# Kernel tuning notes

Measured on AMD Instinct MI355X. Metric: run time of the kernel, lower is better.

Reference implementation:

```python
import jax, jax.numpy as jnp
import numpy as np

H = 8
D = 512
DK = D // H  # 64
ALPHA = 0.2  # leaky relu negative slope


def setup_inputs() -> dict:
    key = jax.random.key(0)
    ks = jax.random.split(key, 10)
    B, N = 8, 1024
    query = jax.random.normal(ks[0], (B, N, D), dtype=jnp.float32)
    key_t = jax.random.normal(ks[1], (B, N, D), dtype=jnp.float32)
    value = jax.random.normal(ks[2], (B, N, D), dtype=jnp.float32)
    mask = jax.random.randint(ks[3], (B, N, N), 0, 2, dtype=jnp.int32)
    scale = 0.02
    Wq = jax.random.normal(ks[4], (D, D), dtype=jnp.float32) * scale
    Wk = jax.random.normal(ks[5], (D, D), dtype=jnp.float32) * scale
    Wv = jax.random.normal(ks[6], (D, D), dtype=jnp.float32) * scale
    Wo = jax.random.normal(ks[7], (D, D), dtype=jnp.float32) * scale
    bq = jnp.zeros((D,), jnp.float32)
    bk = jnp.zeros((D,), jnp.float32)
    bv = jnp.zeros((D,), jnp.float32)
    bo = jnp.zeros((D,), jnp.float32)
    # xavier-uniform-like init for the attention vector a: shape (h, 2*d_k)
    limit = float(np.sqrt(6.0 / (H + 2 * DK)))
    a = jax.random.uniform(ks[8], (H, 2 * DK), dtype=jnp.float32, minval=-limit, maxval=limit)
    return {"query": query, "key": key_t, "value": value, "mask": mask,
            "Wq": Wq, "bq": bq, "Wk": Wk, "bk": bk, "Wv": Wv, "bv": bv,
            "Wo": Wo, "bo": bo, "a": a}


def reference(query, key, value, mask, Wq, bq, Wk, bk, Wv, bv, Wo, bo, a):
    B, N, _ = query.shape

    def proj(x, W, b):
        # torch Linear: x @ W.T + b, then split heads -> (B, H, N, DK)
        return (x @ W.T + b).reshape(B, N, H, DK).transpose(0, 2, 1, 3)

    q = proj(query, Wq, bq)
    k = proj(key, Wk, bk)
    v = proj(value, Wv, bv)

    # 'cat' attention: scores[b,h,i,j] = concat(q_i, k_j) . a[h]
    #                = q_i . a[h,:DK] + k_j . a[h,DK:]  (algebraic decomposition,
    #                 avoids the O(N^2 * 2*DK) concat tensor of the torch code)
    sq = jnp.einsum('bhnd,hd->bhn', q, a[:, :DK])
    sk = jnp.einsum('bhnd,hd->bhn', k, a[:, DK:])
    scores = sq[:, :, :, None] + sk[:, :, None, :]  # (B, H, N, N)

    # mask == 0 -> -inf (mask broadcast over heads), applied BEFORE leaky relu
    scores = jnp.where(mask[:, None, :, :] == 0, -jnp.inf, scores)
    # leaky relu (leaky_relu(-inf) == -inf, preserved)
    scores = jnp.where(scores >= 0, scores, ALPHA * scores)

    p = jax.nn.softmax(scores, axis=-1)
    # fully-masked rows produce NaN -> replace with 0 (as in the torch code)
    p = jnp.where(jnp.isnan(p), jnp.zeros_like(p), p)

    x = jnp.einsum('bhnm,bhmd->bhnd', p, v)
    x = x.transpose(0, 2, 1, 3).reshape(B, N, D)
    return x @ Wo.T + bo
```

## Files before the change

### kernel.cpp

```cpp
#include <hip/hip_runtime.h>
#include <hip/hip_bf16.h>
#include <stdint.h>


typedef __attribute__((ext_vector_type(8))) short short8;
typedef __attribute__((ext_vector_type(4))) float f32x4;

#define LB __launch_bounds__(256)

union U8 { unsigned u[4]; short8 s; uint4 v; };
union U2 { unsigned u[2]; uint2 v; };

__device__ __forceinline__ unsigned short f2bf(float f) {
  unsigned int u = __float_as_uint(f);
  u += 0x7fffu + ((u >> 16) & 1u);
  return (unsigned short)(u >> 16);
}

__device__ __forceinline__ unsigned cvt_pk(float a, float b) {
  unsigned r;
  asm("v_cvt_pk_bf16_f32 %0, %1, %2" : "=v"(r) : "v"(a), "v"(b));
  return r;
}

__device__ __forceinline__ void async_cp16(const void* g, void* l) {
  __builtin_amdgcn_global_load_lds(
      (const __attribute__((address_space(1))) unsigned int*)g,
      (__attribute__((address_space(3))) unsigned int*)l, 16, 0, 0);
}

__global__ LB void prep_kernel(const float* __restrict__ Wv, const float* __restrict__ Wo,
                               unsigned short* __restrict__ wv16, unsigned short* __restrict__ wo16,
                               const float* __restrict__ Wq, const float* __restrict__ Wk,
                               const float* __restrict__ a, const float* __restrict__ bq,
                               const float* __restrict__ bk,
                               unsigned short* __restrict__ Bfrag, float* __restrict__ qkb) {
  const int blk = blockIdx.x, tid = threadIdx.x;
  if (blk < 512) {
    const float* src = blk < 256 ? Wv : Wo;
    unsigned short* dst = blk < 256 ? wv16 : wo16;
    const int idx = ((blk & 255) * 256 + tid) * 4;
    const float4 v = *(const float4*)(src + idx);
    U2 pk;
    pk.u[0] = cvt_pk(v.x, v.y);
    pk.u[1] = cvt_pk(v.z, v.w);
    *(uint2*)(dst + idx) = pk.v;
    return;
  }
  const int t = (blk - 512) * 256 + tid;
  const int d = t & 511, h = t >> 9;
  float aq = 0.f, ak = 0.f;
#pragma unroll 4
  for (int dk = 0; dk < 64; ++dk) {
    aq += Wq[(size_t)(h * 64 + dk) * 512 + d] * a[h * 128 + dk];
    ak += Wk[(size_t)(h * 64 + dk) * 512 + d] * a[h * 128 + 64 + dk];
  }
  const float L2E = 1.4426950408889634f;
  const int ks = d >> 5, lch = (d >> 3) & 3, tt = d & 7;
  Bfrag[((ks * 64 + (lch << 4) + h) << 3) + tt] = f2bf(aq * L2E);
  Bfrag[((ks * 64 + (lch << 4) + 8 + h) << 3) + tt] = f2bf(ak * L2E);
  if (d == 0) {
    float s1 = 0.f, s2 = 0.f;
    for (int dk = 0; dk < 64; ++dk) {
      s1 += bq[h * 64 + dk] * a[h * 128 + dk];
      s2 += bk[h * 64 + dk] * a[h * 128 + 64 + dk];
    }
    qkb[h] = s1 * L2E;
    qkb[8 + h] = s2 * L2E;
  }
}

__global__ LB void mid_kernel(const float* __restrict__ query, const float* __restrict__ key,
                              const unsigned short* __restrict__ Bfrag,
                              const float* __restrict__ qkb,
                              float* __restrict__ sq, float* __restrict__ sk,
                              const float* __restrict__ value,
                              const unsigned short* __restrict__ wv16,
                              const float* __restrict__ bvb, unsigned short* __restrict__ vt,
                              const int* __restrict__ mask, unsigned int* __restrict__ bits) {
  __shared__ char sm[20480];
  const int tid = threadIdx.x, w = tid >> 6, l = tid & 63;
  const int lr = l & 15, lc = l >> 4;
  const int bid = blockIdx.x;
  if (bid >= 1536) {
    unsigned char* nb = (unsigned char*)sm;
    const size_t e0 = ((size_t)(bid - 1536) * 256 + tid) * 4;
    const int4 m = *(const int4*)(mask + e0);
    nb[tid] = (unsigned char)((m.x != 0) | ((m.y != 0) << 1) | ((m.z != 0) << 2) | ((m.w != 0) << 3));
    __syncthreads();
    if (tid < 32) {
      const uint2 p = *(const uint2*)(nb + tid * 8);
      const unsigned lo = p.x, hi = p.y;
      const unsigned wl = (lo & 0xFu) | ((lo >> 4) & 0xF0u) | ((lo >> 8) & 0xF00u) | ((lo >> 12) & 0xF000u);
      const unsigned wh = (hi & 0xFu) | ((hi >> 4) & 0xF0u) | ((hi >> 8) & 0xF00u) | ((hi >> 12) & 0xF000u);
      bits[(bid - 1536) * 32 + tid] = wl | (wh << 16);
    }
    return;
  }
  if (bid >= 1024) {
    float* comb = (float*)sm;
    const int m0 = (bid - 1024) * 16;
    const int k0 = w * 128;
    short8 bf[4];
#pragma unroll
    for (int ks = 0; ks < 4; ++ks)
      bf[ks] = *(const short8*)(Bfrag + (((w * 4 + ks) * 64 + l) << 3));
    const float* qbase = query + (size_t)(m0 + lr) * 512 + k0 + (lc << 3);
    const float* kbase = key + (size_t)(m0 + lr) * 512 + k0 + (lc << 3);
    f32x4 cq = {}, ck = {};
#pragma unroll
    for (int ks = 0; ks < 4; ++ks) {
      const float4 q0 = *(const float4*)(qbase + ks * 32);
      const float4 q1 = *(const float4*)(qbase + ks * 32 + 4);
      const float4 k0v = *(const float4*)(kbase + ks * 32);
      const float4 k1v = *(const float4*)(kbase + ks * 32 + 4);
      U8 aq, ak;
      aq.u[0] = cvt_pk(q0.x, q0.y); aq.u[1] = cvt_pk(q0.z, q0.w);
      aq.u[2] = cvt_pk(q1.x, q1.y); aq.u[3] = cvt_pk(q1.z, q1.w);
      ak.u[0] = cvt_pk(k0v.x, k0v.y); ak.u[1] = cvt_pk(k0v.z, k0v.w);
      ak.u[2] = cvt_pk(k1v.x, k1v.y); ak.u[3] = cvt_pk(k1v.z, k1v.w);
      cq = __builtin_amdgcn_mfma_f32_16x16x32_bf16(aq.s, bf[ks], cq, 0, 0, 0);
      ck = __builtin_amdgcn_mfma_f32_16x16x32_bf16(ak.s, bf[ks], ck, 0, 0, 0);
    }
    if (w) {
      float* p = comb + ((w - 1) * 64 + l) * 9;
#pragma unroll
      for (int r = 0; r < 4; ++r) { p[r] = cq[r]; p[4 + r] = ck[r]; }
    }
    __syncthreads();
    if (w == 0) {
#pragma unroll
      for (int j = 0; j < 3; ++j) {
        const float* p = comb + (j * 64 + l) * 9;
#pragma unroll
        for (int r = 0; r < 4; ++r) { cq[r] += p[r]; ck[r] += p[4 + r]; }
      }
      const int col = l & 15;
      const int mbase = m0 + (lc << 2);
      const int b = mbase >> 10;
      const float bia = qkb[col];
      if (col < 8) {
        float* out = sq + ((size_t)b * 8 + col) * 1024;
#pragma unroll
        for (int r = 0; r < 4; ++r) out[(mbase + r) & 1023] = cq[r] + bia;
      } else {
        float* out = sk + ((size_t)b * 8 + (col - 8)) * 1024;
#pragma unroll
        for (int r = 0; r < 4; ++r) out[(mbase + r) & 1023] = ck[r] + bia;
      }
    }
    return;
  }
  unsigned short* As = (unsigned short*)sm;
  unsigned short* Bs = (unsigned short*)(sm + 4096);
  const int bm = bid >> 2, bn = bid & 3;
  const int m0 = bm * 32, n0 = bn * 128;
  const int wr = (w & 1) * 16, wc = (w >> 1) * 64;
  const int rch = (lc ^ ((lr >> 1) & 3)) << 3;
  const int arow = (w << 3) + (l >> 3);
  const int akc = l & 7;
  const float* asrc = value + (size_t)(m0 + arow) * 512 + (akc << 2);
  const int ach = ((akc >> 1) ^ ((arow >> 1) & 3));
  const int aoff = arow * 32 + (ach << 3) + ((akc & 1) << 2);
  const int crow = l >> 2;
  const int brow0 = (w << 4) + crow, brow1 = ((w + 4) << 4) + crow;
  const unsigned short* bsrc0 = wv16 + (size_t)(n0 + brow0) * 512 + (((l & 3) ^ ((brow0 >> 1) & 3)) << 3);
  const unsigned short* bsrc1 = wv16 + (size_t)(n0 + brow1) * 512 + (((l & 3) ^ ((brow1 >> 1) & 3)) << 3);

  f32x4 acc[4] = {};
  float4 areg = *(const float4*)(asrc);
  async_cp16(bsrc0, Bs + (w << 9));
  async_cp16(bsrc1, Bs + ((w + 4) << 9));
  {
    U2 aw;
    aw.u[0] = cvt_pk(areg.x, areg.y);
    aw.u[1] = cvt_pk(areg.z, areg.w);
    *(uint2*)(As + aoff) = aw.v;
  }
  areg = *(const float4*)(asrc + 32);
  async_cp16(bsrc0 + 32, Bs + 4096 + (w << 9));
  async_cp16(bsrc1 + 32, Bs + 4096 + ((w + 4) << 9));
  asm volatile("s_waitcnt vmcnt(3)" ::: "memory");
  asm volatile("s_waitcnt lgkmcnt(0)" ::: "memory");
  __builtin_amdgcn_sched_barrier(0);
  __builtin_amdgcn_s_barrier();
  int buf = 0;
  for (int kt = 0; kt < 16; ++kt) {
    const short8 af = *(const short8*)(As + (buf << 10) + (wr + lr) * 32 + rch);
    __builtin_amdgcn_s_setprio(1);
#pragma unroll
    for (int j = 0; j < 4; ++j) {
      const short8 bfr = *(const short8*)(Bs + (buf << 12) + (wc + j * 16 + lr) * 32 + rch);
      acc[j] = __builtin_amdgcn_mfma_f32_16x16x32_bf16(af, bfr, acc[j], 0, 0, 0);
    }
    __builtin_amdgcn_s_setprio(0);
    __builtin_amdgcn_s_barrier();
    if (kt < 15) {
      U2 aw;
      aw.u[0] = cvt_pk(areg.x, areg.y);
      aw.u[1] = cvt_pk(areg.z, areg.w);
      *(uint2*)(As + ((buf ^ 1) << 10) + aoff) = aw.v;
      if (kt < 14) {
        areg = *(const float4*)(asrc + (kt + 2) * 32);
        async_cp16(bsrc0 + (kt + 2) * 32, Bs + (buf << 12) + (w << 9));
        async_cp16(bsrc1 + (kt + 2) * 32, Bs + (buf << 12) + ((w + 4) << 9));
        asm volatile("s_waitcnt vmcnt(3)" ::: "memory");
      } else {
        asm volatile("s_waitcnt vmcnt(0)" ::: "memory");
      }
      asm volatile("s_waitcnt lgkmcnt(0)" ::: "memory");
      __builtin_amdgcn_sched_barrier(0);
      __builtin_amdgcn_s_barrier();
    }
    buf ^= 1;
  }
#pragma unroll
  for (int j = 0; j < 4; ++j) {
    const int nn = n0 + wc + j * 16 + lr;
    const float bia = bvb[nn];
    const int mm0 = m0 + wr + lc * 4;
    const int b = mm0 >> 10, t0 = mm0 & 1023;
    const int h = nn >> 6, dk = nn & 63;
    U2 pk;
    pk.u[0] = cvt_pk(acc[j][0] + bia, acc[j][1] + bia);
    pk.u[1] = cvt_pk(acc[j][2] + bia, acc[j][3] + bia);
    *(uint2*)(vt + (((size_t)((b * 8 + h) * 64 + dk)) << 10) + t0) = pk.v;
  }
}

template <int BB16>
__global__ LB void gemm_bt(const unsigned short* __restrict__ A,
                           const void* __restrict__ Bwp,
                           const float* __restrict__ bias, float* __restrict__ outp) {
  __shared__ unsigned short As[2][32 * 32];
  __shared__ unsigned short Bs[2][128 * 32];
  const int tid = threadIdx.x;
  const int w = tid >> 6, l = tid & 63;
  const int lr = l & 15, lc = l >> 4;
  const int bm = blockIdx.x >> 2, bn = blockIdx.x & 3;
  const int m0 = bm * 32, n0 = bn * 128;
  const int wr = (w & 1) * 16, wc = (w >> 1) * 64;
  const int rch = (lc ^ ((lr >> 1) & 3)) << 3;
  const int arow = (w << 3) + (l >> 2);
  const int asc = (l & 3) ^ ((arow >> 1) & 3);
  const unsigned short* asrc = A + (size_t)(m0 + arow) * 512 + (asc << 3);
  const int crow = l >> 2;
  const unsigned short* b16 = (const unsigned short*)Bwp;
  const float* b32 = (const float*)Bwp;
  const int brow0 = (w << 4) + crow, brow1 = ((w + 4) << 4) + crow;
  const unsigned short* bsrc0 = b16 + (size_t)(n0 + brow0) * 512 + (((l & 3) ^ ((brow0 >> 1) & 3)) << 3);
  const unsigned short* bsrc1 = b16 + (size_t)(n0 + brow1) * 512 + (((l & 3) ^ ((brow1 >> 1) & 3)) << 3);

  f32x4 acc[4] = {};
  if (BB16) {
    if (l < 32) async_cp16(asrc, As[0] + (w << 8));
    async_cp16(bsrc0, Bs[0] + (w << 9));
    async_cp16(bsrc1, Bs[0] + ((w + 4) << 9));
    int buf = 0;
    for (int kt = 0; kt < 16; ++kt) {
      if (kt < 15) {
        const int k1 = (kt + 1) * 32;
        if (l < 32) async_cp16(asrc + k1, As[buf ^ 1] + (w << 8));
        async_cp16(bsrc0 + k1, Bs[buf ^ 1] + (w << 9));
        async_cp16(bsrc1 + k1, Bs[buf ^ 1] + ((w + 4) << 9));
        asm volatile("s_waitcnt vmcnt(3)" ::: "memory");
      } else {
        asm volatile("s_waitcnt vmcnt(0)" ::: "memory");
      }
      __builtin_amdgcn_sched_barrier(0);
      __builtin_amdgcn_s_barrier();
      const short8 af = *(const short8*)(As[buf] + (wr + lr) * 32 + rch);
      __builtin_amdgcn_s_setprio(1);
#pragma unroll
      for (int j = 0; j < 4; ++j) {
        const short8 bfr = *(const short8*)(Bs[buf] + (wc + j * 16 + lr) * 32 + rch);
        acc[j] = __builtin_amdgcn_mfma_f32_16x16x32_bf16(af, bfr, acc[j], 0, 0, 0);
      }
      __builtin_amdgcn_s_setprio(0);
      if (kt < 15) __builtin_amdgcn_s_barrier();
      buf ^= 1;
    }
  } else {
    for (int kt = 0; kt < 16; ++kt) {
      const int k0 = kt * 32;
      if (kt) __syncthreads();
      if (l < 32) async_cp16(asrc + k0, As[0] + (w << 8));
#pragma unroll
      for (int it = 0; it < 2; ++it) {
        const int idx = it * 256 + tid;
        const int row = idx >> 2, gr = idx & 3;
        const int sch = (gr ^ ((row >> 1) & 3)) << 3;
        const float4* src = (const float4*)(b32 + (size_t)(n0 + row) * 512 + k0 + gr * 8);
        const float4 b0 = src[0], b1 = src[1];
        U8 t8;
        t8.u[0] = cvt_pk(b0.x, b0.y); t8.u[1] = cvt_pk(b0.z, b0.w);
        t8.u[2] = cvt_pk(b1.x, b1.y); t8.u[3] = cvt_pk(b1.z, b1.w);
        *(uint4*)(Bs[0] + row * 32 + sch) = t8.v;
      }
      __syncthreads();
      const short8 af = *(const short8*)(As[0] + (wr + lr) * 32 + rch);
#pragma unroll
      for (int j = 0; j < 4; ++j) {
        const short8 bfr = *(const short8*)(Bs[0] + (wc + j * 16 + lr) * 32 + rch);
        acc[j] = __builtin_amdgcn_mfma_f32_16x16x32_bf16(af, bfr, acc[j], 0, 0, 0);
      }
    }
  }
#pragma unroll
  for (int j = 0; j < 4; ++j) {
    const int nn = n0 + wc + j * 16 + lr;
    const float bia = bias[nn];
    const int mm0 = m0 + wr + lc * 4;
#pragma unroll
    for (int r = 0; r < 4; ++r)
      outp[(size_t)(mm0 + r) * 512 + nn] = acc[j][r] + bia;
  }
}

__global__ LB void attn_kernel(const float* __restrict__ sq, const float* __restrict__ sk,
                               const unsigned char* __restrict__ mbits,
                               const unsigned short* __restrict__ vt,
                               unsigned short* __restrict__ xb) {
  __shared__ char smem[53248];
  unsigned short* vts = (unsigned short*)smem;
  float* sks = (float*)(smem + 32768);
  char* mks = smem + 36864;
  const int tid = threadIdx.x;
  const int w = tid >> 6, l = tid & 63;
  const int lr = l & 15, lc = l >> 4;
  const int bid = blockIdx.x;
  const int bh = bid & 63, iblk = bid >> 6;
  const int b = bh >> 3, h = bh & 7;
  const int i0b = iblk << 7;
  const int rh = w & 1, jh = w >> 1;
  const int j0 = jh << 9;
  const float* sqp = sq + (size_t)bh * 1024;
  const float* skp = sk + (size_t)bh * 1024;
  const unsigned short* vtp = vt + ((size_t)bh << 16);
  const unsigned char* mrow = mbits + ((size_t)b << 17);

  async_cp16(skp + (w << 8) + l * 4, sks + (w << 8));
#pragma unroll
  for (int m = 0; m < 4; ++m) {
    const int row = (w << 5) + (m << 3) + (l >> 3);
    const int c = (l & 7) ^ (row & 7);
    async_cp16(mrow + (size_t)(i0b + row) * 128 + (c << 4), mks + (w << 12) + (m << 10));
  }
  const int stl = l >> 2;
  const int stc = (l & 3) ^ ((stl >> 1) & 3);
  const unsigned short* vsrc = vtp + stl * 1024 + j0 + (stc << 3);
#define STAGE(bf_, jb_)                                                        \
  {                                                                            \
    unsigned short* d_ = vts + (w << 12) + ((bf_) << 11);                      \
    const unsigned short* s_ = vsrc + (jb_);                                   \
    async_cp16(s_, d_);                                                        \
    async_cp16(s_ + 16384, d_ + 512);                                          \
    async_cp16(s_ + 32768, d_ + 1024);                                         \
    async_cp16(s_ + 49152, d_ + 1536);                                         \
  }
  STAGE(0, 0);
  float sq8[4];
#pragma unroll
  for (int t = 0; t < 4; ++t) sq8[t] = sqp[i0b + (rh << 6) + (t << 4) + lr];
  __syncthreads();

  f32x4 acc[4][4] = {};
  f32x4 accs[4] = {};
  short8 ones;
#pragma unroll
  for (int t = 0; t < 8; ++t) ones[t] = (short)0x3f80;
  const int rx = (lr & 7) << 4;
  const int vread = (lc ^ ((lr >> 1) & 3)) << 3;

  int buf = 0;
  for (int s = 0; s < 16; ++s) {
    if (s < 15) {
      STAGE(buf ^ 1, (s + 1) << 5);
      asm volatile("s_waitcnt vmcnt(4)" ::: "memory");
    } else {
      asm volatile("s_waitcnt vmcnt(0)" ::: "memory");
    }
    __builtin_amdgcn_sched_barrier(0);
    const int jb = j0 + (s << 5);
    const int qb = (jb >> 3) + lc;
    const f32x4 s0 = *(const f32x4*)(sks + jb + (lc << 3));
    const f32x4 s1 = *(const f32x4*)(sks + jb + (lc << 3) + 4);
    U8 pa[4];
#pragma unroll
    for (int t = 0; t < 4; ++t) {
      const int row = (rh << 6) + (t << 4) + lr;
      const unsigned mb = (unsigned char)mks[(row << 7) + (qb ^ rx)];
      const float sqv = sq8[t];
      float e[8];
#pragma unroll
      for (int u = 0; u < 8; ++u) {
        float sv = sqv + (u < 4 ? s0[u] : s1[u - 4]);
        sv = fmaxf(sv, 0.2f * sv);
        const float ex = __builtin_amdgcn_exp2f(sv);
        e[u] = (mb & (1u << u)) ? ex : 0.0f;
      }
      pa[t].u[0] = cvt_pk(e[0], e[1]); pa[t].u[1] = cvt_pk(e[2], e[3]);
      pa[t].u[2] = cvt_pk(e[4], e[5]); pa[t].u[3] = cvt_pk(e[6], e[7]);
    }
    const unsigned short* vbb = vts + (w << 12) + (buf << 11) + vread;
    __builtin_amdgcn_s_setprio(1);
#pragma unroll
    for (int c = 0; c < 4; ++c) {
      const short8 bv = *(const short8*)(vbb + ((c << 4) + lr) * 32);
#pragma unroll
      for (int t = 0; t < 4; ++t)
        acc[t][c] = __builtin_amdgcn_mfma_f32_16x16x32_bf16(pa[t].s, bv, acc[t][c], 0, 0, 0);
    }
#pragma unroll
    for (int t = 0; t < 4; ++t)
      accs[t] = __builtin_amdgcn_mfma_f32_16x16x32_bf16(pa[t].s, ones, accs[t], 0, 0, 0);
    __builtin_amdgcn_s_setprio(0);
    buf ^= 1;
  }
#undef STAGE

  __syncthreads();
  float* cmb = (float*)smem;
  if (jh == 1) {
    float* p = cmb + ((rh << 6) + l) * 84;
#pragma unroll
    for (int t = 0; t < 4; ++t) {
#pragma unroll
      for (int c = 0; c < 4; ++c) *(f32x4*)(p + (t * 4 + c) * 4) = acc[t][c];
      *(f32x4*)(p + 64 + t * 4) = accs[t];
    }
  }
  __syncthreads();
  if (jh == 0) {
    const float* p = cmb + ((rh << 6) + l) * 84;
#pragma unroll
    for (int t = 0; t < 4; ++t) {
#pragma unroll
      for (int c = 0; c < 4; ++c) {
        const f32x4 v = *(const f32x4*)(p + (t * 4 + c) * 4);
#pragma unroll
        for (int r = 0; r < 4; ++r) acc[t][c][r] += v[r];
      }
      const f32x4 vs = *(const f32x4*)(p + 64 + t * 4);
#pragma unroll
      for (int r = 0; r < 4; ++r) accs[t][r] += vs[r];
    }
#pragma unroll
    for (int t = 0; t < 4; ++t) {
#pragma unroll
      for (int r = 0; r < 4; ++r) {
        const float sv = accs[t][r];
        const float inv = sv > 0.0f ? 1.0f / sv : 0.0f;
        const int i = i0b + (rh << 6) + (t << 4) + (lc << 2) + r;
#pragma unroll
        for (int c = 0; c < 4; ++c)
          xb[(((size_t)(b * 1024 + i)) << 9) + h * 64 + (c << 4) + lr] =
              f2bf(acc[t][c][r] * inv);
      }
    }
  }
}

extern "C" void kernel_launch(void* const* d_in, const int* in_sizes, int n_in,
                              void* d_out, int out_size, void* d_ws, size_t ws_size,
                              hipStream_t stream) {
  const float* query = (const float*)d_in[0];
  const float* key   = (const float*)d_in[1];
  const float* value = (const float*)d_in[2];
  const int*   mask  = (const int*)d_in[3];
  const float* Wq = (const float*)d_in[4];
  const float* bq = (const float*)d_in[5];
  const float* Wk = (const float*)d_in[6];
  const float* bk = (const float*)d_in[7];
  const float* Wv = (const float*)d_in[8];
  const float* bv = (const float*)d_in[9];
  const float* Wo = (const float*)d_in[10];
  const float* bo = (const float*)d_in[11];
  const float* a  = (const float*)d_in[12];

  char* oc = (char*)d_out;
  unsigned short* vt = (unsigned short*)(oc + 0);
  unsigned int* mbits = (unsigned int*)(oc + 8388608);
  float* sqv = (float*)(oc + 9437184);
  float* skv = (float*)(oc + 9699328);
  unsigned short* Bfrag = (unsigned short*)(oc + 9961472);
  float* qkb = (float*)(oc + 9977856);
  unsigned short* wv16 = (unsigned short*)(oc + 10485760);
  unsigned short* xb = (unsigned short*)d_ws;

  const bool roomy = ws_size >= 8912896;
  unsigned short* wo16 = roomy ? (unsigned short*)((char*)d_ws + 8388608) : (unsigned short*)(oc + 11010048);

  prep_kernel<<<528, 256, 0, stream>>>(Wv, Wo, wv16, wo16, Wq, Wk, a, bq, bk, Bfrag, qkb);
  mid_kernel<<<9728, 256, 0, stream>>>(query, key, Bfrag, qkb, sqv, skv,
                                       value, wv16, bv, vt, mask, mbits);
  attn_kernel<<<512, 256, 0, stream>>>(sqv, skv, (const unsigned char*)mbits, vt, xb);
  if (roomy)
    gemm_bt<1><<<1024, 256, 0, stream>>>(xb, (const void*)wo16, bo, (float*)d_out);
  else
    gemm_bt<0><<<1024, 256, 0, stream>>>(xb, (const void*)Wo, bo, (float*)d_out);
}
```

Baseline: 81.23 us.

## Split attention blocks to 64 query rows with 4-way key split and tree reduction

Each attention block now handles 64 query rows instead of 128, and each of the four waves covers a quarter of the key dimension instead of half. The grid doubles to 1024 blocks and LDS use per block drops, which should fill more CUs and raise occupancy on the 256-CU part. The price is a two-level cross-wave reduction with extra LDS traffic and barriers, plus more redundant loads of the V tiles across blocks.

```diff
diff --git a/kernel.cpp b/kernel.cpp
--- a/kernel.cpp
+++ b/kernel.cpp
@@ -321,7 +321,7 @@
                                const unsigned char* __restrict__ mbits,
                                const unsigned short* __restrict__ vt,
                                unsigned short* __restrict__ xb) {
-  __shared__ char smem[53248];
+  __shared__ char smem[45056];
   unsigned short* vts = (unsigned short*)smem;
   float* sks = (float*)(smem + 32768);
   char* mks = smem + 36864;
@@ -331,9 +331,8 @@
   const int bid = blockIdx.x;
   const int bh = bid & 63, iblk = bid >> 6;
   const int b = bh >> 3, h = bh & 7;
-  const int i0b = iblk << 7;
-  const int rh = w & 1, jh = w >> 1;
-  const int j0 = jh << 9;
+  const int i0b = iblk << 6;
+  const int j0 = w << 8;
   const float* sqp = sq + (size_t)bh * 1024;
   const float* skp = sk + (size_t)bh * 1024;
   const unsigned short* vtp = vt + ((size_t)bh << 16);
@@ -341,10 +340,10 @@
 
   async_cp16(skp + (w << 8) + l * 4, sks + (w << 8));
 #pragma unroll
-  for (int m = 0; m < 4; ++m) {
-    const int row = (w << 5) + (m << 3) + (l >> 3);
+  for (int m = 0; m < 2; ++m) {
+    const int row = (w << 4) + (m << 3) + (l >> 3);
     const int c = (l & 7) ^ (row & 7);
-    async_cp16(mrow + (size_t)(i0b + row) * 128 + (c << 4), mks + (w << 12) + (m << 10));
+    async_cp16(mrow + (size_t)(i0b + row) * 128 + (c << 4), mks + (w << 11) + (m << 10));
   }
   const int stl = l >> 2;
   const int stc = (l & 3) ^ ((stl >> 1) & 3);
@@ -361,7 +360,7 @@
   STAGE(0, 0);
   float sq8[4];
 #pragma unroll
-  for (int t = 0; t < 4; ++t) sq8[t] = sqp[i0b + (rh << 6) + (t << 4) + lr];
+  for (int t = 0; t < 4; ++t) sq8[t] = sqp[i0b + (t << 4) + lr];
   __syncthreads();
 
   f32x4 acc[4][4] = {};
@@ -373,8 +372,8 @@
   const int vread = (lc ^ ((lr >> 1) & 3)) << 3;
 
   int buf = 0;
-  for (int s = 0; s < 16; ++s) {
-    if (s < 15) {
+  for (int s = 0; s < 8; ++s) {
+    if (s < 7) {
       STAGE(buf ^ 1, (s + 1) << 5);
       asm volatile("s_waitcnt vmcnt(4)" ::: "memory");
     } else {
@@ -388,7 +387,7 @@
     U8 pa[4];
 #pragma unroll
     for (int t = 0; t < 4; ++t) {
-      const int row = (rh << 6) + (t << 4) + lr;
+      const int row = (t << 4) + lr;
       const unsigned mb = (unsigned char)mks[(row << 7) + (qb ^ rx)];
       const float sqv = sq8[t];
       float e[8];
@@ -421,37 +420,44 @@
 
   __syncthreads();
   float* cmb = (float*)smem;
-  if (jh == 1) {
-    float* p = cmb + ((rh << 6) + l) * 84;
-#pragma unroll
-    for (int t = 0; t < 4; ++t) {
-#pragma unroll
-      for (int c = 0; c < 4; ++c) *(f32x4*)(p + (t * 4 + c) * 4) = acc[t][c];
-      *(f32x4*)(p + 64 + t * 4) = accs[t];
-    }
-  }
+#define CMB_W(B_)                                                              \
+  {                                                                            \
+    float* p = cmb + ((B_) * 64 + l) * 85;                                     \
+    _Pragma("unroll") for (int t = 0; t < 4; ++t) {                            \
+      _Pragma("unroll") for (int c = 0; c < 4; ++c)                            \
+          *(f32x4*)(p + (t * 4 + c) * 4) = acc[t][c];                          \
+      *(f32x4*)(p + 64 + t * 4) = accs[t];                                     \
+    }                                                                          \
+  }
+#define CMB_A(B_)                                                              \
+  {                                                                            \
+    const float* p = cmb + ((B_) * 64 + l) * 85;                               \
+    _Pragma("unroll") for (int t = 0; t < 4; ++t) {                            \
+      _Pragma("unroll") for (int c = 0; c < 4; ++c) {                          \
+        const f32x4 v = *(const f32x4*)(p + (t * 4 + c) * 4);                  \
+        _Pragma("unroll") for (int r = 0; r < 4; ++r) acc[t][c][r] += v[r];    \
+      }                                                                        \
+      const f32x4 vs = *(const f32x4*)(p + 64 + t * 4);                        \
+      _Pragma("unroll") for (int r = 0; r < 4; ++r) accs[t][r] += vs[r];       \
+    }                                                                          \
+  }
+  if (w == 1) CMB_W(0);
+  if (w == 3) CMB_W(1);
   __syncthreads();
-  if (jh == 0) {
-    const float* p = cmb + ((rh << 6) + l) * 84;
-#pragma unroll
-    for (int t = 0; t < 4; ++t) {
-#pragma unroll
-      for (int c = 0; c < 4; ++c) {
-        const f32x4 v = *(const f32x4*)(p + (t * 4 + c) * 4);
-#pragma unroll
-        for (int r = 0; r < 4; ++r) acc[t][c][r] += v[r];
-      }
-      const f32x4 vs = *(const f32x4*)(p + 64 + t * 4);
-#pragma unroll
-      for (int r = 0; r < 4; ++r) accs[t][r] += vs[r];
-    }
+  if (w == 0) CMB_A(0);
+  if (w == 2) CMB_A(1);
+  __syncthreads();
+  if (w == 2) CMB_W(0);
+  __syncthreads();
+  if (w == 0) {
+    CMB_A(0);
 #pragma unroll
     for (int t = 0; t < 4; ++t) {
 #pragma unroll
       for (int r = 0; r < 4; ++r) {
         const float sv = accs[t][r];
         const float inv = sv > 0.0f ? 1.0f / sv : 0.0f;
-        const int i = i0b + (rh << 6) + (t << 4) + (lc << 2) + r;
+        const int i = i0b + (t << 4) + (lc << 2) + r;
 #pragma unroll
         for (int c = 0; c < 4; ++c)
           xb[(((size_t)(b * 1024 + i)) << 9) + h * 64 + (c << 4) + lr] =
@@ -459,6 +465,8 @@
       }
     }
   }
+#undef CMB_W
+#undef CMB_A
 }
 
 extern "C" void kernel_launch(void* const* d_in, const int* in_sizes, int n_in,
@@ -494,7 +502,7 @@
   prep_kernel<<<528, 256, 0, stream>>>(Wv, Wo, wv16, wo16, Wq, Wk, a, bq, bk, Bfrag, qkb);
   mid_kernel<<<9728, 256, 0, stream>>>(query, key, Bfrag, qkb, sqv, skv,
                                        value, wv16, bv, vt, mask, mbits);
-  attn_kernel<<<512, 256, 0, stream>>>(sqv, skv, (const unsigned char*)mbits, vt, xb);
+  attn_kernel<<<1024, 256, 0, stream>>>(sqv, skv, (const unsigned char*)mbits, vt, xb);
   if (roomy)
     gemm_bt<1><<<1024, 256, 0, stream>>>(xb, (const void*)wo16, bo, (float*)d_out);
   else
```

After: 90.86 us. 1.12x slower.

## Split attention key range across eight waves with register-resident V and serial reduction

Applied to the files above, without the earlier changes.

The attention kernel now launches twice as many blocks of 512 threads, each covering 64 query rows, with every wave owning a 128-key slice. V fragments are loaded straight from global memory into registers, replacing the double-buffered LDS pipeline, so shared memory per block falls from 52KB to 21KB and occupancy should rise. The partial accumulators from the eight waves are summed through a serial loop of seven LDS write/read rounds, each with two block barriers. This adds synchronization and duplicated sq/mask work, and the register V tile adds register pressure.

```diff
diff --git a/kernel.cpp b/kernel.cpp
--- a/kernel.cpp
+++ b/kernel.cpp
@@ -7,6 +7,7 @@
 typedef __attribute__((ext_vector_type(4))) float f32x4;
 
 #define LB __launch_bounds__(256)
+#define LB512 __launch_bounds__(512)
 
 union U8 { unsigned u[4]; short8 s; uint4 v; };
 union U2 { unsigned u[2]; uint2 v; };
@@ -317,51 +318,41 @@
   }
 }
 
-__global__ LB void attn_kernel(const float* __restrict__ sq, const float* __restrict__ sk,
-                               const unsigned char* __restrict__ mbits,
-                               const unsigned short* __restrict__ vt,
-                               unsigned short* __restrict__ xb) {
-  __shared__ char smem[53248];
-  unsigned short* vts = (unsigned short*)smem;
-  float* sks = (float*)(smem + 32768);
-  char* mks = smem + 36864;
+__global__ LB512 void attn_kernel(const float* __restrict__ sq, const float* __restrict__ sk,
+                                  const unsigned char* __restrict__ mbits,
+                                  const unsigned short* __restrict__ vt,
+                                  unsigned short* __restrict__ xb) {
+  __shared__ char smem[21504];
+  float* sks = (float*)smem;
+  char* mks = smem + 4096;
   const int tid = threadIdx.x;
   const int w = tid >> 6, l = tid & 63;
   const int lr = l & 15, lc = l >> 4;
   const int bid = blockIdx.x;
   const int bh = bid & 63, iblk = bid >> 6;
   const int b = bh >> 3, h = bh & 7;
-  const int i0b = iblk << 7;
-  const int rh = w & 1, jh = w >> 1;
-  const int j0 = jh << 9;
+  const int i0b = iblk << 6;
+  const int j0 = w << 7;
   const float* sqp = sq + (size_t)bh * 1024;
   const float* skp = sk + (size_t)bh * 1024;
   const unsigned short* vtp = vt + ((size_t)bh << 16);
   const unsigned char* mrow = mbits + ((size_t)b << 17);
 
-  async_cp16(skp + (w << 8) + l * 4, sks + (w << 8));
-#pragma unroll
-  for (int m = 0; m < 4; ++m) {
-    const int row = (w << 5) + (m << 3) + (l >> 3);
+  if (w < 4) async_cp16(skp + (w << 8) + l * 4, sks + (w << 8));
+  {
+    const int row = (w << 3) + (l >> 3);
     const int c = (l & 7) ^ (row & 7);
-    async_cp16(mrow + (size_t)(i0b + row) * 128 + (c << 4), mks + (w << 12) + (m << 10));
-  }
-  const int stl = l >> 2;
-  const int stc = (l & 3) ^ ((stl >> 1) & 3);
-  const unsigned short* vsrc = vtp + stl * 1024 + j0 + (stc << 3);
-#define STAGE(bf_, jb_)                                                        \
-  {                                                                            \
-    unsigned short* d_ = vts + (w << 12) + ((bf_) << 11);                      \
-    const unsigned short* s_ = vsrc + (jb_);                                   \
-    async_cp16(s_, d_);                                                        \
-    async_cp16(s_ + 16384, d_ + 512);                                          \
-    async_cp16(s_ + 32768, d_ + 1024);                                         \
-    async_cp16(s_ + 49152, d_ + 1536);                                         \
-  }
-  STAGE(0, 0);
+    async_cp16(mrow + (size_t)(i0b + row) * 128 + (c << 4), mks + (w << 10));
+  }
+  short8 vrb[4][4];
+#pragma unroll
+  for (int c = 0; c < 4; ++c)
+#pragma unroll
+    for (int s = 0; s < 4; ++s)
+      vrb[c][s] = *(const short8*)(vtp + (size_t)(c * 16 + lr) * 1024 + j0 + s * 32 + (lc << 3));
   float sq8[4];
 #pragma unroll
-  for (int t = 0; t < 4; ++t) sq8[t] = sqp[i0b + (rh << 6) + (t << 4) + lr];
+  for (int t = 0; t < 4; ++t) sq8[t] = sqp[i0b + (t << 4) + lr];
   __syncthreads();
 
   f32x4 acc[4][4] = {};
@@ -370,17 +361,9 @@
 #pragma unroll
   for (int t = 0; t < 8; ++t) ones[t] = (short)0x3f80;
   const int rx = (lr & 7) << 4;
-  const int vread = (lc ^ ((lr >> 1) & 3)) << 3;
-
-  int buf = 0;
-  for (int s = 0; s < 16; ++s) {
-    if (s < 15) {
-      STAGE(buf ^ 1, (s + 1) << 5);
-      asm volatile("s_waitcnt vmcnt(4)" ::: "memory");
-    } else {
-      asm volatile("s_waitcnt vmcnt(0)" ::: "memory");
-    }
-    __builtin_amdgcn_sched_barrier(0);
+
+#pragma unroll
+  for (int s = 0; s < 4; ++s) {
     const int jb = j0 + (s << 5);
     const int qb = (jb >> 3) + lc;
     const f32x4 s0 = *(const f32x4*)(sks + jb + (lc << 3));
@@ -388,7 +371,7 @@
     U8 pa[4];
 #pragma unroll
     for (int t = 0; t < 4; ++t) {
-      const int row = (rh << 6) + (t << 4) + lr;
+      const int row = (t << 4) + lr;
       const unsigned mb = (unsigned char)mks[(row << 7) + (qb ^ rx)];
       const float sqv = sq8[t];
       float e[8];
@@ -402,56 +385,57 @@
       pa[t].u[0] = cvt_pk(e[0], e[1]); pa[t].u[1] = cvt_pk(e[2], e[3]);
       pa[t].u[2] = cvt_pk(e[4], e[5]); pa[t].u[3] = cvt_pk(e[6], e[7]);
     }
-    const unsigned short* vbb = vts + (w << 12) + (buf << 11) + vread;
     __builtin_amdgcn_s_setprio(1);
 #pragma unroll
-    for (int c = 0; c < 4; ++c) {
-      const short8 bv = *(const short8*)(vbb + ((c << 4) + lr) * 32);
+    for (int c = 0; c < 4; ++c)
 #pragma unroll
       for (int t = 0; t < 4; ++t)
-        acc[t][c] = __builtin_amdgcn_mfma_f32_16x16x32_bf16(pa[t].s, bv, acc[t][c], 0, 0, 0);
-    }
+        acc[t][c] = __builtin_amdgcn_mfma_f32_16x16x32_bf16(pa[t].s, vrb[c][s], acc[t][c], 0, 0, 0);
 #pragma unroll
     for (int t = 0; t < 4; ++t)
       accs[t] = __builtin_amdgcn_mfma_f32_16x16x32_bf16(pa[t].s, ones, accs[t], 0, 0, 0);
     __builtin_amdgcn_s_setprio(0);
-    buf ^= 1;
-  }
-#undef STAGE
-
+  }
+
+  float* cmb = (float*)smem;
   __syncthreads();
-  float* cmb = (float*)smem;
-  if (jh == 1) {
-    float* p = cmb + ((rh << 6) + l) * 84;
-#pragma unroll
-    for (int t = 0; t < 4; ++t) {
-#pragma unroll
-      for (int c = 0; c < 4; ++c) *(f32x4*)(p + (t * 4 + c) * 4) = acc[t][c];
-      *(f32x4*)(p + 64 + t * 4) = accs[t];
-    }
-  }
-  __syncthreads();
-  if (jh == 0) {
-    const float* p = cmb + ((rh << 6) + l) * 84;
-#pragma unroll
-    for (int t = 0; t < 4; ++t) {
-#pragma unroll
-      for (int c = 0; c < 4; ++c) {
-        const f32x4 v = *(const f32x4*)(p + (t * 4 + c) * 4);
-#pragma unroll
-        for (int r = 0; r < 4; ++r) acc[t][c][r] += v[r];
-      }
-      const f32x4 vs = *(const f32x4*)(p + 64 + t * 4);
-#pragma unroll
-      for (int r = 0; r < 4; ++r) accs[t][r] += vs[r];
-    }
+#pragma unroll 1
+  for (int src = 1; src < 8; ++src) {
+    if (w == src) {
+      float* p = cmb + l * 81;
+#pragma unroll
+      for (int t = 0; t < 4; ++t) {
+#pragma unroll
+        for (int c = 0; c < 4; ++c) *(f32x4*)(p + (t * 4 + c) * 4) = acc[t][c];
+        *(f32x4*)(p + 64 + t * 4) = accs[t];
+      }
+    }
+    __syncthreads();
+    if (w == 0) {
+      const float* p = cmb + l * 81;
+#pragma unroll
+      for (int t = 0; t < 4; ++t) {
+#pragma unroll
+        for (int c = 0; c < 4; ++c) {
+          const f32x4 v = *(const f32x4*)(p + (t * 4 + c) * 4);
+#pragma unroll
+          for (int r = 0; r < 4; ++r) acc[t][c][r] += v[r];
+        }
+        const f32x4 vs = *(const f32x4*)(p + 64 + t * 4);
+#pragma unroll
+        for (int r = 0; r < 4; ++r) accs[t][r] += vs[r];
+      }
+    }
+    __syncthreads();
+  }
+  if (w == 0) {
 #pragma unroll
     for (int t = 0; t < 4; ++t) {
 #pragma unroll
       for (int r = 0; r < 4; ++r) {
         const float sv = accs[t][r];
         const float inv = sv > 0.0f ? 1.0f / sv : 0.0f;
-        const int i = i0b + (rh << 6) + (t << 4) + (lc << 2) + r;
+        const int i = i0b + (t << 4) + (lc << 2) + r;
 #pragma unroll
         for (int c = 0; c < 4; ++c)
           xb[(((size_t)(b * 1024 + i)) << 9) + h * 64 + (c << 4) + lr] =
@@ -494,7 +478,7 @@
   prep_kernel<<<528, 256, 0, stream>>>(Wv, Wo, wv16, wo16, Wq, Wk, a, bq, bk, Bfrag, qkb);
   mid_kernel<<<9728, 256, 0, stream>>>(query, key, Bfrag, qkb, sqv, skv,
                                        value, wv16, bv, vt, mask, mbits);
-  attn_kernel<<<512, 256, 0, stream>>>(sqv, skv, (const unsigned char*)mbits, vt, xb);
+  attn_kernel<<<1024, 512, 0, stream>>>(sqv, skv, (const unsigned char*)mbits, vt, xb);
   if (roomy)
     gemm_bt<1><<<1024, 256, 0, stream>>>(xb, (const void*)wo16, bo, (float*)d_out);
   else
```

Result: slower. 126.1 us (+55.2%).

## Share V tiles between wave pairs and stage 64-column slabs per iteration

Applied to the files above, without the earlier changes.

V staging moves from a private per-wave buffer to a buffer shared by the two waves with the same j-half. Each wave loads half of the 64 dk rows for a 64-column slab, and a new XOR swizzle avoids LDS bank conflicts. Each outer iteration now covers two 32-column sub-steps, which halves the number of pipeline stages and cuts redundant global V traffic per block. In exchange it adds two workgroup barriers per slab, since the buffer is shared across waves, and these can stall waves that would otherwise run independently.

```diff
diff --git a/kernel.cpp b/kernel.cpp
--- a/kernel.cpp
+++ b/kernel.cpp
@@ -346,17 +346,18 @@
     const int c = (l & 7) ^ (row & 7);
     async_cp16(mrow + (size_t)(i0b + row) * 128 + (c << 4), mks + (w << 12) + (m << 10));
   }
-  const int stl = l >> 2;
-  const int stc = (l & 3) ^ ((stl >> 1) & 3);
-  const unsigned short* vsrc = vtp + stl * 1024 + j0 + (stc << 3);
-#define STAGE(bf_, jb_)                                                        \
+  const int sdk = l >> 3;
+  const int c0 = (l & 7) ^ sdk;
+  const unsigned short* vsA = vtp + (size_t)((rh << 5) + sdk) * 1024 + j0 + (c0 << 3);
+  const unsigned short* vsB = vtp + (size_t)((rh << 5) + sdk) * 1024 + j0 + ((c0 ^ 4) << 3);
+  unsigned short* vdst = vts + (jh << 13) + ((rh << 5) << 6);
+#define STAGE(bf_, jsl_)                                                       \
   {                                                                            \
-    unsigned short* d_ = vts + (w << 12) + ((bf_) << 11);                      \
-    const unsigned short* s_ = vsrc + (jb_);                                   \
-    async_cp16(s_, d_);                                                        \
-    async_cp16(s_ + 16384, d_ + 512);                                          \
-    async_cp16(s_ + 32768, d_ + 1024);                                         \
-    async_cp16(s_ + 49152, d_ + 1536);                                         \
+    unsigned short* d_ = vdst + ((bf_) << 12);                                 \
+    async_cp16(vsA + (jsl_), d_);                                              \
+    async_cp16(vsB + 8192 + (jsl_), d_ + 512);                                 \
+    async_cp16(vsA + 16384 + (jsl_), d_ + 1024);                               \
+    async_cp16(vsB + 24576 + (jsl_), d_ + 1536);                               \
   }
   STAGE(0, 0);
   float sq8[4];
@@ -370,51 +371,57 @@
 #pragma unroll
   for (int t = 0; t < 8; ++t) ones[t] = (short)0x3f80;
   const int rx = (lr & 7) << 4;
-  const int vread = (lc ^ ((lr >> 1) & 3)) << 3;
+  const int pxor = (lr & 7) ^ (((lr >> 3) & 1) << 2);
 
   int buf = 0;
-  for (int s = 0; s < 16; ++s) {
-    if (s < 15) {
-      STAGE(buf ^ 1, (s + 1) << 5);
+  for (int slab = 0; slab < 8; ++slab) {
+    if (slab < 7) {
+      STAGE(buf ^ 1, (slab + 1) << 6);
       asm volatile("s_waitcnt vmcnt(4)" ::: "memory");
     } else {
       asm volatile("s_waitcnt vmcnt(0)" ::: "memory");
     }
     __builtin_amdgcn_sched_barrier(0);
-    const int jb = j0 + (s << 5);
-    const int qb = (jb >> 3) + lc;
-    const f32x4 s0 = *(const f32x4*)(sks + jb + (lc << 3));
-    const f32x4 s1 = *(const f32x4*)(sks + jb + (lc << 3) + 4);
-    U8 pa[4];
-#pragma unroll
-    for (int t = 0; t < 4; ++t) {
-      const int row = (rh << 6) + (t << 4) + lr;
-      const unsigned mb = (unsigned char)mks[(row << 7) + (qb ^ rx)];
-      const float sqv = sq8[t];
-      float e[8];
-#pragma unroll
-      for (int u = 0; u < 8; ++u) {
-        float sv = sqv + (u < 4 ? s0[u] : s1[u - 4]);
-        sv = fmaxf(sv, 0.2f * sv);
-        const float ex = __builtin_amdgcn_exp2f(sv);
-        e[u] = (mb & (1u << u)) ? ex : 0.0f;
-      }
-      pa[t].u[0] = cvt_pk(e[0], e[1]); pa[t].u[1] = cvt_pk(e[2], e[3]);
-      pa[t].u[2] = cvt_pk(e[4], e[5]); pa[t].u[3] = cvt_pk(e[6], e[7]);
-    }
-    const unsigned short* vbb = vts + (w << 12) + (buf << 11) + vread;
-    __builtin_amdgcn_s_setprio(1);
-#pragma unroll
-    for (int c = 0; c < 4; ++c) {
-      const short8 bv = *(const short8*)(vbb + ((c << 4) + lr) * 32);
+    __builtin_amdgcn_s_barrier();
+#pragma unroll
+    for (int s2 = 0; s2 < 2; ++s2) {
+      const int jb = j0 + (slab << 6) + (s2 << 5);
+      const int qb = (jb >> 3) + lc;
+      const f32x4 s0 = *(const f32x4*)(sks + jb + (lc << 3));
+      const f32x4 s1 = *(const f32x4*)(sks + jb + (lc << 3) + 4);
+      U8 pa[4];
+#pragma unroll
+      for (int t = 0; t < 4; ++t) {
+        const int row = (rh << 6) + (t << 4) + lr;
+        const unsigned mb = (unsigned char)mks[(row << 7) + (qb ^ rx)];
+        const float sqv = sq8[t];
+        float e[8];
+#pragma unroll
+        for (int u = 0; u < 8; ++u) {
+          float sv = sqv + (u < 4 ? s0[u] : s1[u - 4]);
+          sv = fmaxf(sv, 0.2f * sv);
+          const float ex = __builtin_amdgcn_exp2f(sv);
+          e[u] = (mb & (1u << u)) ? ex : 0.0f;
+        }
+        pa[t].u[0] = cvt_pk(e[0], e[1]); pa[t].u[1] = cvt_pk(e[2], e[3]);
+        pa[t].u[2] = cvt_pk(e[4], e[5]); pa[t].u[3] = cvt_pk(e[6], e[7]);
+      }
+      const unsigned short* vbb = vts + (jh << 13) + (buf << 12)
+                                + ((((s2 << 2) + lc) ^ pxor) << 3);
+      __builtin_amdgcn_s_setprio(1);
+#pragma unroll
+      for (int c = 0; c < 4; ++c) {
+        const short8 bv = *(const short8*)(vbb + (((c << 4) + lr) << 6));
+#pragma unroll
+        for (int t = 0; t < 4; ++t)
+          acc[t][c] = __builtin_amdgcn_mfma_f32_16x16x32_bf16(pa[t].s, bv, acc[t][c], 0, 0, 0);
+      }
 #pragma unroll
       for (int t = 0; t < 4; ++t)
-        acc[t][c] = __builtin_amdgcn_mfma_f32_16x16x32_bf16(pa[t].s, bv, acc[t][c], 0, 0, 0);
-    }
-#pragma unroll
-    for (int t = 0; t < 4; ++t)
-      accs[t] = __builtin_amdgcn_mfma_f32_16x16x32_bf16(pa[t].s, ones, accs[t], 0, 0, 0);
-    __builtin_amdgcn_s_setprio(0);
+        accs[t] = __builtin_amdgcn_mfma_f32_16x16x32_bf16(pa[t].s, ones, accs[t], 0, 0, 0);
+      __builtin_amdgcn_s_setprio(0);
+    }
+    if (slab < 7) __builtin_amdgcn_s_barrier();
     buf ^= 1;
   }
 #undef STAGE
```

After: 81.97 us. About the same (+0.9%).
